# Kernel tuning notes

Measured on AMD Instinct MI355X. Metric: run time of the kernel, lower is better.

Reference implementation:

```python
import jax, jax.numpy as jnp
import numpy as np

HIDDEN = 2048
NUM_HEADS = 16
HEAD_DIM = HIDDEN // NUM_HEADS  # 128
B, S = 2, 2048


def setup_inputs() -> dict:
    key = jax.random.key(0)
    ks = jax.random.split(key, 16)
    w = lambda k, shp: (jax.random.normal(k, shp, jnp.float32) * 0.02)
    return {
        "query": jax.random.normal(ks[0], (B, S, HIDDEN), jnp.float32),
        "key": jax.random.normal(ks[1], (B, S, HIDDEN), jnp.float32),
        "value": jax.random.normal(ks[2], (B, S, HIDDEN), jnp.float32),
        "Wq": w(ks[3], (HIDDEN, HIDDEN)), "bq": jnp.zeros((HIDDEN,), jnp.float32),
        "Wk": w(ks[4], (HIDDEN, HIDDEN)), "bk": jnp.zeros((HIDDEN,), jnp.float32),
        "Wv": w(ks[5], (HIDDEN, HIDDEN)), "bv": jnp.zeros((HIDDEN,), jnp.float32),
        "Wo": w(ks[6], (HIDDEN, HIDDEN)), "bo": jnp.zeros((HIDDEN,), jnp.float32),
        "Wf1": w(ks[7], (HEAD_DIM, 2 * HEAD_DIM)), "bf1": jnp.zeros((2 * HEAD_DIM,), jnp.float32),
        "Wf2": w(ks[8], (2 * HEAD_DIM, HEAD_DIM)), "bf2": jnp.zeros((HEAD_DIM,), jnp.float32),
    }


def reference(query, key, value, Wq, bq, Wk, bk, Wv, bv, Wo, bo, Wf1, bf1, Wf2, bf2):
    b, s, _ = query.shape

    def split_heads(x):  # [b,s,H] -> [b,h,s,d]
        return x.reshape(b, s, NUM_HEADS, HEAD_DIM).transpose(0, 2, 1, 3)

    def feature_map(x):  # MLP on last dim: d -> 2d -> relu -> d
        return jax.nn.relu(x @ Wf1 + bf1) @ Wf2 + bf2

    Q = feature_map(split_heads(query @ Wq + bq))
    K = feature_map(split_heads(key @ Wk + bk))
    V = split_heads(value @ Wv + bv)

    # K^T V per head: [b,h,d,e]
    KV = jnp.einsum("bhsd,bhse->bhde", K, V)
    QKV = jnp.einsum("bhsd,bhde->bhse", Q, KV)
    # denominator: sum of all K entries per (b,h) -> scalar per head
    denom = jnp.sum(K, axis=(-2, -1), keepdims=True) + 1e-8
    QKV = QKV / denom

    context = QKV.transpose(0, 2, 1, 3).reshape(b, s, HIDDEN)
    output = context @ Wo + bo

    attn_weights = jnp.full((b, NUM_HEADS, s, s), 1.0 / s, dtype=query.dtype)
    return output, attn_weights
```

## Files before the change

kernel.cpp:

```cpp
#include <hip/hip_runtime.h>


typedef __bf16 bf16_t;
typedef __bf16 bf16x8 __attribute__((ext_vector_type(8)));
typedef __bf16 bf16x4 __attribute__((ext_vector_type(4)));
typedef float  f32x4  __attribute__((ext_vector_type(4)));

#define FILLV (1.0f / 2048.0f)

#define VMCNT2() asm volatile("s_waitcnt vmcnt(2)" ::: "memory")
#define VMCNT0() asm volatile("s_waitcnt vmcnt(0)" ::: "memory")
#define LGKM0()  asm volatile("s_waitcnt lgkmcnt(0)" ::: "memory")
#define BAR()    __builtin_amdgcn_s_barrier()
#define SCHED0() __builtin_amdgcn_sched_barrier(0)

__device__ __forceinline__ void gload16(const void* g, void* l) {
  __builtin_amdgcn_global_load_lds(
      (__attribute__((address_space(1))) void*)(g),
      (__attribute__((address_space(3))) void*)(l), 16, 0, 0);
}

__device__ __forceinline__ void stage_half(const bf16_t* __restrict__ g,
                                           int h, unsigned char* ldsT, int t) {
  const bf16_t* gh = g + (long)h * 128 * 2048;
  unsigned char* lh = ldsT + h * 16384;
#pragma unroll
  for (int i = 0; i < 2; ++i) {
    const int c = t + i * 512;
    const int r = c >> 3;
    const int cc = ((c & 7) ^ (r & 7)) * 8;
    gload16(gh + (long)r * 2048 + cc, lh + c * 16);
  }
}

__device__ __forceinline__ bf16x8 lds_frag(const unsigned char* base,
                                           int row, int kelem) {
  int byte = row * 128 + kelem * 2;
  byte ^= (row & 7) << 4;
  return *(const bf16x8*)(base + byte);
}

template<bool OUTF32, bool TRIPLE>
__global__ __launch_bounds__(512, 2) void gemm8(
    const bf16_t* __restrict__ A, const bf16_t* __restrict__ Wt,
    const float* __restrict__ b0, const float* __restrict__ b1,
    const float* __restrict__ b2, void* __restrict__ C,
    float* __restrict__ attn, long fillBase)
{
  __shared__ __align__(16) unsigned char smem[98304];
  const int t = threadIdx.x;
  const int lane = t & 63;
  const int wid = t >> 6;
  const int wr = wid >> 2, wc = wid & 3;
  const int bid = blockIdx.x;
  const int nby = gridDim.x >> 4;
  const int by = bid % nby, bx = bid / nby;
  const int which = TRIPLE ? (by >> 4) : 0;
  const bf16_t* Ab = A + (long)by * 256 * 2048;
  const bf16_t* Bb = Wt + (long)which * 4194304 + (long)bx * 128 * 2048;
  const float* bias = TRIPLE ? (which == 0 ? b0 : (which == 1 ? b1 : b2)) : b0;

  const int lr = lane & 15;
  const int l8 = (lane >> 4) * 8;
  const f32x4 fv = {FILLV, FILLV, FILLV, FILLV};
  const int nblk = gridDim.x;

  f32x4 acc[8][2];
#pragma unroll
  for (int i = 0; i < 8; ++i)
#pragma unroll
    for (int j = 0; j < 2; ++j) acc[i][j] = (f32x4){0.f, 0.f, 0.f, 0.f};

  stage_half(Ab, 0, smem, t);
  stage_half(Ab, 1, smem, t);
  stage_half(Bb, 0, smem + 32768, t);

  bf16x8 aF[4][2], bF[2][2];

  for (int kt = 0; kt < 32; ++kt) {
    const int cur = kt & 1;
    unsigned char* curA = smem + cur * 49152;
    unsigned char* curB = curA + 32768;
    unsigned char* nxtA = smem + (cur ^ 1) * 49152;
    unsigned char* nxtB = nxtA + 32768;
    const bool hn = kt < 31;
    const bf16_t* An = Ab + (kt + 1) * 64;
    const bf16_t* Bn = Bb + (kt + 1) * 64;
    const int arow = wr * 128 + lr;
    const int brow = wc * 32 + lr;
    f32x4* fillp = (f32x4*)attn + fillBase + ((long)kt * nblk + bid) * 1024 + t;

    if (hn) { stage_half(An, 0, nxtA, t); VMCNT2(); }
    else    { VMCNT0(); }
    BAR();
#pragma unroll
    for (int mi = 0; mi < 4; ++mi)
#pragma unroll
      for (int kk = 0; kk < 2; ++kk)
        aF[mi][kk] = lds_frag(curA, arow + mi * 16, kk * 32 + l8);
#pragma unroll
    for (int kk = 0; kk < 2; ++kk)
      bF[0][kk] = lds_frag(curB, brow, kk * 32 + l8);
    LGKM0(); SCHED0();
    __builtin_amdgcn_s_setprio(1);
#pragma unroll
    for (int mi = 0; mi < 4; ++mi)
#pragma unroll
      for (int kk = 0; kk < 2; ++kk)
        acc[mi][0] = __builtin_amdgcn_mfma_f32_16x16x32_bf16(
            aF[mi][kk], bF[0][kk], acc[mi][0], 0, 0, 0);
    __builtin_amdgcn_s_setprio(0);
    BAR();

    if (hn) stage_half(An, 1, nxtA, t);
    __builtin_nontemporal_store(fv, fillp);
#pragma unroll
    for (int kk = 0; kk < 2; ++kk)
      bF[1][kk] = lds_frag(curB, brow + 16, kk * 32 + l8);
    BAR(); LGKM0(); SCHED0();
    __builtin_amdgcn_s_setprio(1);
#pragma unroll
    for (int mi = 0; mi < 4; ++mi)
#pragma unroll
      for (int kk = 0; kk < 2; ++kk)
        acc[mi][1] = __builtin_amdgcn_mfma_f32_16x16x32_bf16(
            aF[mi][kk], bF[1][kk], acc[mi][1], 0, 0, 0);
    __builtin_amdgcn_s_setprio(0);
    BAR();

    if (hn) stage_half(Bn, 0, nxtB, t);
    __builtin_nontemporal_store(fv, fillp + 512);
#pragma unroll
    for (int mi = 0; mi < 4; ++mi)
#pragma unroll
      for (int kk = 0; kk < 2; ++kk)
        aF[mi][kk] = lds_frag(curA, arow + 64 + mi * 16, kk * 32 + l8);
    BAR(); LGKM0(); SCHED0();
    __builtin_amdgcn_s_setprio(1);
#pragma unroll
    for (int mi = 0; mi < 4; ++mi)
#pragma unroll
      for (int kk = 0; kk < 2; ++kk)
        acc[4 + mi][0] = __builtin_amdgcn_mfma_f32_16x16x32_bf16(
            aF[mi][kk], bF[0][kk], acc[4 + mi][0], 0, 0, 0);
    __builtin_amdgcn_s_setprio(0);
    BAR();

    BAR(); SCHED0();
    __builtin_amdgcn_s_setprio(1);
#pragma unroll
    for (int mi = 0; mi < 4; ++mi)
#pragma unroll
      for (int kk = 0; kk < 2; ++kk)
        acc[4 + mi][1] = __builtin_amdgcn_mfma_f32_16x16x32_bf16(
            aF[mi][kk], bF[1][kk], acc[4 + mi][1], 0, 0, 0);
    __builtin_amdgcn_s_setprio(0);
    BAR();
  }

  const int row0g = by * 256 + wr * 128;
  const int col0g = bx * 128 + wc * 32;
  float* lw = (float*)smem + wid * 2304;
#pragma unroll
  for (int p = 0; p < 2; ++p) {
    LGKM0();
#pragma unroll
    for (int mi = 0; mi < 4; ++mi)
#pragma unroll
      for (int ni = 0; ni < 2; ++ni) {
        const float bvv = bias[col0g + ni * 16 + lr];
#pragma unroll
        for (int j = 0; j < 4; ++j) {
          const int rl = mi * 16 + (lane >> 4) * 4 + j;
          lw[rl * 36 + ni * 16 + lr] = acc[p * 4 + mi][ni][j] + bvv;
        }
      }
    LGKM0(); SCHED0();
#pragma unroll
    for (int i = 0; i < 8; ++i) {
      const int c = i * 64 + lane;
      const int rl = c >> 3, cc = (c & 7) * 4;
      f32x4 v4 = *(const f32x4*)&lw[rl * 36 + cc];
      const long gaddr = (long)(row0g + p * 64 + rl) * 2048 + col0g + cc;
      if (OUTF32) {
        *(f32x4*)&((float*)C)[gaddr] = v4;
      } else {
        bf16x4 o = {(bf16_t)v4[0], (bf16_t)v4[1],
                    (bf16_t)v4[2], (bf16_t)v4[3]};
        *(bf16x4*)&((bf16_t*)C)[gaddr] = o;
      }
    }
  }
}

__global__ __launch_bounds__(256) void gemm_bt(
    const bf16_t* __restrict__ A, const bf16_t* __restrict__ Bt,
    bf16_t* __restrict__ C, int K, int lda, int ldb, int ldc,
    long aBatchB, long aBatchH, long bBatchB, long bBatchH,
    long cBatchB, long cBatchH, int HperB)
{
  __shared__ bf16_t As[128 * 64];
  __shared__ bf16_t Bs[128 * 64];

  const int z  = blockIdx.z;
  const int zb = z / HperB, zh = z % HperB;
  const bf16_t* Ab = A  + (long)zb * aBatchB + (long)zh * aBatchH
                        + (long)blockIdx.y * 128 * lda;
  const bf16_t* Bb = Bt + (long)zb * bBatchB + (long)zh * bBatchH
                        + (long)blockIdx.x * 128 * ldb;

  const int t = threadIdx.x;
  const int lane = t & 63, w = t >> 6;
  const int wm = (w >> 1) * 64, wn = (w & 1) * 64;

  f32x4 acc[4][4];
#pragma unroll
  for (int i = 0; i < 4; ++i)
#pragma unroll
    for (int j = 0; j < 4; ++j) acc[i][j] = (f32x4){0.f, 0.f, 0.f, 0.f};

  for (int k0 = 0; k0 < K; k0 += 64) {
#pragma unroll
    for (int i = 0; i < 4; ++i) {
      int c = i * 256 + t;
      int row = c >> 3, col = (c & 7) * 8;
      gload16(Ab + (long)row * lda + k0 + col, &As[c * 8]);
      gload16(Bb + (long)row * ldb + k0 + col, &Bs[c * 8]);
    }
    __syncthreads();
#pragma unroll
    for (int kk = 0; kk < 2; ++kk) {
      bf16x8 af[4], bfr[4];
#pragma unroll
      for (int mi = 0; mi < 4; ++mi)
        af[mi] = *(const bf16x8*)&As[(wm + mi * 16 + (lane & 15)) * 64
                                     + kk * 32 + (lane >> 4) * 8];
#pragma unroll
      for (int ni = 0; ni < 4; ++ni)
        bfr[ni] = *(const bf16x8*)&Bs[(wn + ni * 16 + (lane & 15)) * 64
                                      + kk * 32 + (lane >> 4) * 8];
#pragma unroll
      for (int mi = 0; mi < 4; ++mi)
#pragma unroll
        for (int ni = 0; ni < 4; ++ni)
          acc[mi][ni] = __builtin_amdgcn_mfma_f32_16x16x32_bf16(
              af[mi], bfr[ni], acc[mi][ni], 0, 0, 0);
    }
    __syncthreads();
  }

  const long cb = (long)zb * cBatchB + (long)zh * cBatchH;
  const int row0 = blockIdx.y * 128 + wm;
  const int col0 = blockIdx.x * 128 + wn;
#pragma unroll
  for (int mi = 0; mi < 4; ++mi) {
#pragma unroll
    for (int ni = 0; ni < 4; ++ni) {
      const int col = col0 + ni * 16 + (lane & 15);
#pragma unroll
      for (int j = 0; j < 4; ++j) {
        const int row = row0 + mi * 16 + (lane >> 4) * 4 + j;
        C[cb + (long)row * ldc + col] = (bf16_t)acc[mi][ni][j];
      }
    }
  }
}

__global__ __launch_bounds__(256) void fm_fused(
    const bf16_t* __restrict__ A, const bf16_t* __restrict__ W1f,
    const bf16_t* __restrict__ W2f, const float* __restrict__ b1,
    const float* __restrict__ b2, bf16_t* __restrict__ Out)
{
  __shared__ __align__(16) unsigned char As_[16384];
  __shared__ char Hs[64 * 256 * 2];
  const int t = threadIdx.x, lane = t & 63, w = t >> 6;
  const long r0 = (long)blockIdx.x * 64;
  const int lr = lane & 15, lk = lane >> 4;

  {
    const bf16_t* Ab = A + r0 * 128;
#pragma unroll
    for (int i = 0; i < 4; ++i) {
      int c = i * 256 + t;
      int r = c >> 4;
      int cc = ((c & 15) ^ (r & 7)) * 8;
      gload16(Ab + (long)r * 128 + cc, As_ + c * 16);
    }
  }
  __syncthreads();

  f32x4 acc[4][4];
#pragma unroll
  for (int i = 0; i < 4; ++i)
#pragma unroll
    for (int j = 0; j < 4; ++j) acc[i][j] = (f32x4){0.f, 0.f, 0.f, 0.f};
  const int wn = w * 64;
#pragma unroll
  for (int kk = 0; kk < 4; ++kk) {
    bf16x8 af[4], bfr[4];
#pragma unroll
    for (int mi = 0; mi < 4; ++mi) {
      const int m = mi * 16 + lr;
      int byte = (m << 8) + kk * 64 + lk * 16;
      byte ^= (m & 7) << 4;
      af[mi] = *(const bf16x8*)(As_ + byte);
    }
#pragma unroll
    for (int ni = 0; ni < 4; ++ni)
      bfr[ni] = *(const bf16x8*)&W1f[((((w << 2) + ni) << 2) + kk) * 512
                                     + lane * 8];
#pragma unroll
    for (int mi = 0; mi < 4; ++mi)
#pragma unroll
      for (int ni = 0; ni < 4; ++ni)
        acc[mi][ni] = __builtin_amdgcn_mfma_f32_16x16x32_bf16(
            af[mi], bfr[ni], acc[mi][ni], 0, 0, 0);
  }
#pragma unroll
  for (int ni = 0; ni < 4; ++ni) {
    const int col = wn + ni * 16 + lr;
    const float bvv = b1[col];
#pragma unroll
    for (int mi = 0; mi < 4; ++mi)
#pragma unroll
      for (int j = 0; j < 4; ++j) {
        const int row = mi * 16 + lk * 4 + j;
        float h = fmaxf(acc[mi][ni][j] + bvv, 0.f);
        int byte = (row << 9) + (col << 1);
        byte ^= (row & 7) << 4;
        *(bf16_t*)(Hs + byte) = (bf16_t)h;
      }
  }
  __syncthreads();

  f32x4 acc2[4][2];
#pragma unroll
  for (int i = 0; i < 4; ++i)
#pragma unroll
    for (int j = 0; j < 2; ++j) acc2[i][j] = (f32x4){0.f, 0.f, 0.f, 0.f};
  const int wn2 = w * 32;
#pragma unroll
  for (int kk = 0; kk < 8; ++kk) {
    bf16x8 af[4], bfr[2];
#pragma unroll
    for (int mi = 0; mi < 4; ++mi) {
      const int m = mi * 16 + lr;
      int byte = (m << 9) + kk * 64 + lk * 16;
      byte ^= (m & 7) << 4;
      af[mi] = *(const bf16x8*)(Hs + byte);
    }
#pragma unroll
    for (int ni = 0; ni < 2; ++ni)
      bfr[ni] = *(const bf16x8*)&W2f[((((w << 1) + ni) << 3) + kk) * 512
                                     + lane * 8];
#pragma unroll
    for (int mi = 0; mi < 4; ++mi)
#pragma unroll
      for (int ni = 0; ni < 2; ++ni)
        acc2[mi][ni] = __builtin_amdgcn_mfma_f32_16x16x32_bf16(
            af[mi], bfr[ni], acc2[mi][ni], 0, 0, 0);
  }
#pragma unroll
  for (int ni = 0; ni < 2; ++ni) {
    const int col = wn2 + ni * 16 + lr;
    const float bvv = b2[col];
#pragma unroll
    for (int mi = 0; mi < 4; ++mi)
#pragma unroll
      for (int j = 0; j < 4; ++j) {
        const int row = mi * 16 + lk * 4 + j;
        Out[(r0 + row) * 128 + col] = (bf16_t)(acc2[mi][ni][j] + bvv);
      }
  }
}

__global__ __launch_bounds__(256) void prep(
    const float* __restrict__ q, const float* __restrict__ k,
    const float* __restrict__ v,
    const float* __restrict__ Wq, const float* __restrict__ Wk,
    const float* __restrict__ Wv, const float* __restrict__ Wo,
    const float* __restrict__ Wf1, const float* __restrict__ Wf2,
    bf16_t* __restrict__ qkv_bf, bf16_t* __restrict__ Wqkv_t,
    bf16_t* __restrict__ Wf1_f, bf16_t* __restrict__ Wf2_f)
{
  const int t = threadIdx.x;
  const int bid = blockIdx.x;
  __shared__ float ts[64 * 65];

  if (bid < 12288) {
    const float* in = bid < 4096 ? q : (bid < 8192 ? k : v);
    bf16_t* o = qkv_bf + (long)(bid >> 12) * 8388608L;
    const long base = (long)(bid & 4095) * 2048 + t * 8;
    float4 x0 = *(const float4*)&in[base];
    float4 x1 = *(const float4*)&in[base + 4];
    bf16x8 r = {(bf16_t)x0.x, (bf16_t)x0.y, (bf16_t)x0.z, (bf16_t)x0.w,
                (bf16_t)x1.x, (bf16_t)x1.y, (bf16_t)x1.z, (bf16_t)x1.w};
    *(bf16x8*)&o[base] = r;
    return;
  }

  if (bid >= 16384) {
    const bool isW2 = (bid == 16385);
    const float* Wsrc = isW2 ? Wf2 : Wf1;
    bf16_t* dst = isW2 ? Wf2_f : Wf1_f;
    const int Nd2 = isW2 ? 128 : 256;
#pragma unroll
    for (int i = 0; i < 16; ++i) {
      const int idx = t * 16 + i;
      const int ln = idx & 63;
      int kk, col;
      if (!isW2) {
        kk = (idx >> 6) & 3;
        const int ni = (idx >> 8) & 3, ww = idx >> 10;
        col = ww * 64 + ni * 16 + (ln & 15);
      } else {
        kk = (idx >> 6) & 7;
        const int ni = (idx >> 9) & 1, ww = idx >> 10;
        col = ww * 32 + ni * 16 + (ln & 15);
      }
      const int krow = kk * 32 + (ln >> 4) * 8;
      bf16x8 vv;
#pragma unroll
      for (int e = 0; e < 8; ++e)
        vv[e] = (bf16_t)Wsrc[(long)(krow + e) * Nd2 + col];
      *(bf16x8*)&dst[(long)idx * 8] = vv;
    }
    return;
  }

  const int tile = bid - 12288;
  const int wsel = tile >> 10, r = tile & 1023;
  const float* W = wsel == 0 ? Wq : wsel == 1 ? Wk : wsel == 2 ? Wv : Wo;
  bf16_t* outp = Wqkv_t + (long)wsel * 4194304L;
  const int k0 = (r >> 5) * 64, n0 = (r & 31) * 64;

#pragma unroll
  for (int i = 0; i < 4; ++i) {
    const int idx = i * 256 + t;
    const int rr = idx >> 4, cc = (idx & 15) * 4;
    float4 x = *(const float4*)&W[(long)(k0 + rr) * 2048 + n0 + cc];
    float* p = &ts[rr * 65 + cc];
    p[0] = x.x; p[1] = x.y; p[2] = x.z; p[3] = x.w;
  }
  __syncthreads();

#pragma unroll
  for (int i = 0; i < 2; ++i) {
    const int idx = i * 256 + t;
    const int n = idx >> 3, kc = (idx & 7) * 8;
    bf16x8 vv;
#pragma unroll
    for (int qq = 0; qq < 8; ++qq) vv[qq] = (bf16_t)ts[(kc + qq) * 65 + n];
    *(bf16x8*)&outp[(long)(n0 + n) * 2048 + k0 + kc] = vv;
  }
}

__global__ __launch_bounds__(256) void kv_partial(
    const bf16_t* __restrict__ Kf, const bf16_t* __restrict__ Vp,
    float* __restrict__ part, float* __restrict__ part_denom) {
  const int z = blockIdx.y, b = z >> 4, h = z & 15;
  const int s0 = blockIdx.x * 256;
  const int t = threadIdx.x;
  __shared__ bf16_t Ks[32 * 128];
  __shared__ bf16_t Vs[32 * 128];
  __shared__ float red[4];
  const bf16_t* Kb = Kf + (long)b * 4194304 + h * 128;
  const bf16_t* Vb = Vp + (long)b * 4194304 + h * 128;
  float acc[8][8];
#pragma unroll
  for (int i = 0; i < 8; ++i)
#pragma unroll
    for (int j = 0; j < 8; ++j) acc[i][j] = 0.f;
  float ksum = 0.f;
  const int d0 = (t & 15) * 8, e0 = (t >> 4) * 8;
  for (int sc = 0; sc < 256; sc += 32) {
#pragma unroll
    for (int i = 0; i < 2; ++i) {
      int idx = (i * 256 + t) * 8;
      int r = idx >> 7, c = idx & 127;
      long g = (long)(s0 + sc + r) * 2048 + c;
      *(bf16x8*)&Ks[r * 128 + c] = *(const bf16x8*)&Kb[g];
      *(bf16x8*)&Vs[r * 128 + c] = *(const bf16x8*)&Vb[g];
    }
    __syncthreads();
    {
      bf16x8 a0 = *(const bf16x8*)&Ks[t * 16];
      bf16x8 a1 = *(const bf16x8*)&Ks[t * 16 + 8];
#pragma unroll
      for (int j = 0; j < 8; ++j) ksum += (float)a0[j] + (float)a1[j];
    }
    for (int s = 0; s < 32; ++s) {
      bf16x8 kv = *(const bf16x8*)&Ks[s * 128 + d0];
      bf16x8 vv = *(const bf16x8*)&Vs[s * 128 + e0];
      float kf[8], vf[8];
#pragma unroll
      for (int i = 0; i < 8; ++i) { kf[i] = (float)kv[i]; vf[i] = (float)vv[i]; }
#pragma unroll
      for (int i = 0; i < 8; ++i)
#pragma unroll
        for (int j = 0; j < 8; ++j) acc[i][j] += vf[i] * kf[j];
    }
    __syncthreads();
  }

#pragma unroll
  for (int off = 32; off; off >>= 1) ksum += __shfl_down(ksum, off, 64);
  if ((t & 63) == 0) red[t >> 6] = ksum;
  __syncthreads();
  if (t == 0)
    part_denom[blockIdx.x * 32 + z] = red[0] + red[1] + red[2] + red[3];

  float* pb = part + ((long)blockIdx.x * 32 + z) * 16384;
#pragma unroll
  for (int i = 0; i < 8; ++i)
#pragma unroll
    for (int j = 0; j < 8; ++j)
      pb[(e0 + i) * 128 + (d0 + j)] = acc[i][j];
}

__global__ __launch_bounds__(256) void kv_reduce(
    const float* __restrict__ part, const float* __restrict__ part_denom,
    bf16_t* __restrict__ KVT) {
  const int z = blockIdx.x >> 4, slice = blockIdx.x & 15;
  const int t = threadIdx.x;
  float dsum = 0.f;
#pragma unroll
  for (int c = 0; c < 8; ++c) dsum += part_denom[c * 32 + z];
  const float inv = 1.0f / (dsum + 1e-8f);
  const long i0 = slice * 1024 + t * 4;
  f32x4 s = {0.f, 0.f, 0.f, 0.f};
#pragma unroll
  for (int c = 0; c < 8; ++c) {
    f32x4 v = *(const f32x4*)&part[((long)c * 32 + z) * 16384 + i0];
    s.x += v.x; s.y += v.y; s.z += v.z; s.w += v.w;
  }
  bf16x4 o = {(bf16_t)(s.x * inv), (bf16_t)(s.y * inv),
              (bf16_t)(s.z * inv), (bf16_t)(s.w * inv)};
  *(bf16x4*)&KVT[(long)z * 16384 + i0] = o;
}

extern "C" void kernel_launch(void* const* d_in, const int* in_sizes, int n_in,
                              void* d_out, int out_size, void* d_ws, size_t ws_size,
                              hipStream_t stream) {
  (void)in_sizes; (void)n_in; (void)out_size; (void)ws_size;
  const float* q   = (const float*)d_in[0];
  const float* k   = (const float*)d_in[1];
  const float* v   = (const float*)d_in[2];
  const float* Wq  = (const float*)d_in[3];
  const float* bq  = (const float*)d_in[4];
  const float* Wk  = (const float*)d_in[5];
  const float* bk  = (const float*)d_in[6];
  const float* Wv  = (const float*)d_in[7];
  const float* bv  = (const float*)d_in[8];
  const float* Wo  = (const float*)d_in[9];
  const float* bo  = (const float*)d_in[10];
  const float* Wf1 = (const float*)d_in[11];
  const float* bf1 = (const float*)d_in[12];
  const float* Wf2 = (const float*)d_in[13];
  const float* bf2 = (const float*)d_in[14];

  bf16_t* P      = (bf16_t*)d_ws;
  bf16_t* qkv_bf = P;
  bf16_t* Wqkv_t = P + 25165824L;
  bf16_t* Wo_t   = P + 37748736L;
  bf16_t* Qp     = P + 42008576L;
  bf16_t* Vp     = P + 58785792L;
  bf16_t* Qf     = P + 83951616L;
  bf16_t* Kf     = P + 92340224L;
  bf16_t* KVT    = P + 100728832L;
  bf16_t* Wf1_f  = P + 101253120L;
  bf16_t* Wf2_f  = P + 101285888L;
  float*  part   = (float*)d_ws;
  float*  part_denom = (float*)d_ws + 4194304L;

  float* out0 = (float*)d_out;
  float* attn = (float*)d_out + 8388608L;

  dim3 blk(256);

  prep<<<16386, blk, 0, stream>>>(q, k, v, Wq, Wk, Wv, Wo, Wf1, Wf2,
                                  qkv_bf, Wqkv_t, Wf1_f, Wf2_f);

  gemm8<false, true><<<768, 512, 0, stream>>>(
      qkv_bf, Wqkv_t, bq, bk, bv, Qp, attn, 0L);

  fm_fused<<<2048, blk, 0, stream>>>(Qp, Wf1_f, Wf2_f, bf1, bf2, Qf);

  kv_partial<<<dim3(8, 32), blk, 0, stream>>>(Kf, Vp, part, part_denom);

  kv_reduce<<<512, blk, 0, stream>>>(part, part_denom, KVT);

  gemm_bt<<<dim3(1, 16, 32), blk, 0, stream>>>(
      Qf, KVT, Vp, 128, 2048, 128, 2048,
      4194304L, 128L, 262144L, 16384L, 4194304L, 128L, 16);

  gemm8<true, false><<<256, 512, 0, stream>>>(
      Vp, Wo_t, bo, nullptr, nullptr, out0, attn, 25165824L);
}
```

Before: 299.8 us.

## Fuse feature-map MLP into QKV projection GEMM epilogue

The QKV projection GEMM and the separate feature-map MLP kernel are merged into one kernel. Q and K tiles (256 tokens × 128 head-dim) stay in LDS, where the two-layer MLP runs directly and the result is written to Qf/Kf. The V tiles keep the plain epilogue. This removes the Qp round trip through global memory and one kernel launch. In exchange, LDS grows to 128KB and launch bounds drop to one block per CU, which lowers occupancy during the main GEMM loop.

```diff
diff --git a/kernel.cpp b/kernel.cpp
--- a/kernel.cpp
+++ b/kernel.cpp
@@ -40,11 +40,273 @@
   return *(const bf16x8*)(base + byte);
 }
 
-template<bool OUTF32, bool TRIPLE>
-__global__ __launch_bounds__(512, 2) void gemm8(
+__global__ __launch_bounds__(512, 1) void proj_fm8(
     const bf16_t* __restrict__ A, const bf16_t* __restrict__ Wt,
-    const float* __restrict__ b0, const float* __restrict__ b1,
-    const float* __restrict__ b2, void* __restrict__ C,
+    const float* __restrict__ bq, const float* __restrict__ bk,
+    const float* __restrict__ bv,
+    const bf16_t* __restrict__ W1f, const bf16_t* __restrict__ W2f,
+    const float* __restrict__ b1, const float* __restrict__ b2,
+    bf16_t* __restrict__ Vp, bf16_t* __restrict__ Qf, bf16_t* __restrict__ Kf,
+    float* __restrict__ attn)
+{
+  __shared__ __align__(16) unsigned char smem[131072];
+  const int t = threadIdx.x;
+  const int lane = t & 63;
+  const int wid = t >> 6;
+  const int wr = wid >> 2, wc = wid & 3;
+  const int bid = blockIdx.x;
+  const int by = bid % 48, bx = bid / 48;
+  const int which = by >> 4;
+  const bf16_t* Ab = A + (long)by * 256 * 2048;
+  const bf16_t* Bb = Wt + (long)which * 4194304 + (long)bx * 128 * 2048;
+  const float* bias = which == 0 ? bq : (which == 1 ? bk : bv);
+
+  const int lr = lane & 15;
+  const int l8 = (lane >> 4) * 8;
+  const f32x4 fv = {FILLV, FILLV, FILLV, FILLV};
+
+  f32x4 acc[8][2];
+#pragma unroll
+  for (int i = 0; i < 8; ++i)
+#pragma unroll
+    for (int j = 0; j < 2; ++j) acc[i][j] = (f32x4){0.f, 0.f, 0.f, 0.f};
+
+  stage_half(Ab, 0, smem, t);
+  stage_half(Ab, 1, smem, t);
+  stage_half(Bb, 0, smem + 32768, t);
+
+  bf16x8 aF[4][2], bF[2][2];
+
+  for (int kt = 0; kt < 32; ++kt) {
+    const int cur = kt & 1;
+    unsigned char* curA = smem + cur * 49152;
+    unsigned char* curB = curA + 32768;
+    unsigned char* nxtA = smem + (cur ^ 1) * 49152;
+    unsigned char* nxtB = nxtA + 32768;
+    const bool hn = kt < 31;
+    const bf16_t* An = Ab + (kt + 1) * 64;
+    const bf16_t* Bn = Bb + (kt + 1) * 64;
+    const int arow = wr * 128 + lr;
+    const int brow = wc * 32 + lr;
+    f32x4* fillp = (f32x4*)attn + ((long)kt * 768 + bid) * 1024 + t;
+
+    if (hn) { stage_half(An, 0, nxtA, t); VMCNT2(); }
+    else    { VMCNT0(); }
+    BAR();
+#pragma unroll
+    for (int mi = 0; mi < 4; ++mi)
+#pragma unroll
+      for (int kk = 0; kk < 2; ++kk)
+        aF[mi][kk] = lds_frag(curA, arow + mi * 16, kk * 32 + l8);
+#pragma unroll
+    for (int kk = 0; kk < 2; ++kk)
+      bF[0][kk] = lds_frag(curB, brow, kk * 32 + l8);
+    LGKM0(); SCHED0();
+    __builtin_amdgcn_s_setprio(1);
+#pragma unroll
+    for (int mi = 0; mi < 4; ++mi)
+#pragma unroll
+      for (int kk = 0; kk < 2; ++kk)
+        acc[mi][0] = __builtin_amdgcn_mfma_f32_16x16x32_bf16(
+            aF[mi][kk], bF[0][kk], acc[mi][0], 0, 0, 0);
+    __builtin_amdgcn_s_setprio(0);
+    BAR();
+
+    if (hn) stage_half(An, 1, nxtA, t);
+    __builtin_nontemporal_store(fv, fillp);
+#pragma unroll
+    for (int kk = 0; kk < 2; ++kk)
+      bF[1][kk] = lds_frag(curB, brow + 16, kk * 32 + l8);
+    BAR(); LGKM0(); SCHED0();
+    __builtin_amdgcn_s_setprio(1);
+#pragma unroll
+    for (int mi = 0; mi < 4; ++mi)
+#pragma unroll
+      for (int kk = 0; kk < 2; ++kk)
+        acc[mi][1] = __builtin_amdgcn_mfma_f32_16x16x32_bf16(
+            aF[mi][kk], bF[1][kk], acc[mi][1], 0, 0, 0);
+    __builtin_amdgcn_s_setprio(0);
+    BAR();
+
+    if (hn) stage_half(Bn, 0, nxtB, t);
+    __builtin_nontemporal_store(fv, fillp + 512);
+#pragma unroll
+    for (int mi = 0; mi < 4; ++mi)
+#pragma unroll
+      for (int kk = 0; kk < 2; ++kk)
+        aF[mi][kk] = lds_frag(curA, arow + 64 + mi * 16, kk * 32 + l8);
+    BAR(); LGKM0(); SCHED0();
+    __builtin_amdgcn_s_setprio(1);
+#pragma unroll
+    for (int mi = 0; mi < 4; ++mi)
+#pragma unroll
+      for (int kk = 0; kk < 2; ++kk)
+        acc[4 + mi][0] = __builtin_amdgcn_mfma_f32_16x16x32_bf16(
+            aF[mi][kk], bF[0][kk], acc[4 + mi][0], 0, 0, 0);
+    __builtin_amdgcn_s_setprio(0);
+    BAR();
+
+    BAR(); SCHED0();
+    __builtin_amdgcn_s_setprio(1);
+#pragma unroll
+    for (int mi = 0; mi < 4; ++mi)
+#pragma unroll
+      for (int kk = 0; kk < 2; ++kk)
+        acc[4 + mi][1] = __builtin_amdgcn_mfma_f32_16x16x32_bf16(
+            aF[mi][kk], bF[1][kk], acc[4 + mi][1], 0, 0, 0);
+    __builtin_amdgcn_s_setprio(0);
+    BAR();
+  }
+
+  const int tokBase = (by & 15) * 256;
+  const int col0 = wc * 32;
+
+  if (which == 2) {
+    float* lw = (float*)smem + wid * 2304;
+#pragma unroll
+    for (int p = 0; p < 2; ++p) {
+      LGKM0();
+#pragma unroll
+      for (int mi = 0; mi < 4; ++mi)
+#pragma unroll
+        for (int ni = 0; ni < 2; ++ni) {
+          const float bvv = bias[bx * 128 + col0 + ni * 16 + lr];
+#pragma unroll
+          for (int j = 0; j < 4; ++j) {
+            const int rl = mi * 16 + (lane >> 4) * 4 + j;
+            lw[rl * 36 + ni * 16 + lr] = acc[p * 4 + mi][ni][j] + bvv;
+          }
+        }
+      LGKM0(); SCHED0();
+#pragma unroll
+      for (int i = 0; i < 8; ++i) {
+        const int c = i * 64 + lane;
+        const int rl = c >> 3, cc = (c & 7) * 4;
+        f32x4 v4 = *(const f32x4*)&lw[rl * 36 + cc];
+        const int tok = tokBase + wr * 128 + p * 64 + rl;
+        bf16x4 o = {(bf16_t)v4[0], (bf16_t)v4[1],
+                    (bf16_t)v4[2], (bf16_t)v4[3]};
+        *(bf16x4*)&Vp[(long)tok * 2048 + bx * 128 + col0 + cc] = o;
+      }
+    }
+    return;
+  }
+
+  unsigned char* Ct = smem;
+  unsigned char* Hs = smem + 65536;
+
+#pragma unroll
+  for (int mi = 0; mi < 8; ++mi)
+#pragma unroll
+    for (int ni = 0; ni < 2; ++ni) {
+      const int col = col0 + ni * 16 + lr;
+      const float bvv = bias[bx * 128 + col];
+#pragma unroll
+      for (int j = 0; j < 4; ++j) {
+        const int row = wr * 128 + mi * 16 + (lane >> 4) * 4 + j;
+        int byte = (row << 8) + (col << 1);
+        byte ^= (row & 7) << 4;
+        *(bf16_t*)(Ct + byte) = (bf16_t)(acc[mi][ni][j] + bvv);
+      }
+    }
+  __syncthreads();
+
+  bf16_t* dst = which == 0 ? Qf : Kf;
+  const int wr2 = wid >> 2, wc2 = wid & 3;
+  const int lk = lane >> 4;
+
+#pragma unroll
+  for (int p = 0; p < 2; ++p) {
+    f32x4 a1[4][4];
+#pragma unroll
+    for (int i = 0; i < 4; ++i)
+#pragma unroll
+      for (int j = 0; j < 4; ++j) a1[i][j] = (f32x4){0.f, 0.f, 0.f, 0.f};
+#pragma unroll
+    for (int kk = 0; kk < 4; ++kk) {
+      bf16x8 af[4], bfr[4];
+#pragma unroll
+      for (int mi = 0; mi < 4; ++mi) {
+        const int row = p * 128 + wr2 * 64 + mi * 16 + lr;
+        int byte = (row << 8) + (kk * 64 + lk * 16);
+        byte ^= (row & 7) << 4;
+        af[mi] = *(const bf16x8*)(Ct + byte);
+      }
+#pragma unroll
+      for (int ni = 0; ni < 4; ++ni)
+        bfr[ni] = *(const bf16x8*)&W1f[((((wc2 << 2) + ni) << 2) + kk) * 512
+                                       + lane * 8];
+#pragma unroll
+      for (int mi = 0; mi < 4; ++mi)
+#pragma unroll
+        for (int ni = 0; ni < 4; ++ni)
+          a1[mi][ni] = __builtin_amdgcn_mfma_f32_16x16x32_bf16(
+              af[mi], bfr[ni], a1[mi][ni], 0, 0, 0);
+    }
+    if (p) __syncthreads();
+#pragma unroll
+    for (int ni = 0; ni < 4; ++ni) {
+      const int col = wc2 * 64 + ni * 16 + lr;
+      const float bvv = b1[col];
+#pragma unroll
+      for (int mi = 0; mi < 4; ++mi)
+#pragma unroll
+        for (int j = 0; j < 4; ++j) {
+          const int row = wr2 * 64 + mi * 16 + lk * 4 + j;
+          float h = fmaxf(a1[mi][ni][j] + bvv, 0.f);
+          int byte = (row << 9) + (col << 1);
+          byte ^= (row & 7) << 4;
+          *(bf16_t*)(Hs + byte) = (bf16_t)h;
+        }
+    }
+    __syncthreads();
+
+    f32x4 a2[4][2];
+#pragma unroll
+    for (int i = 0; i < 4; ++i)
+#pragma unroll
+      for (int j = 0; j < 2; ++j) a2[i][j] = (f32x4){0.f, 0.f, 0.f, 0.f};
+#pragma unroll
+    for (int kk = 0; kk < 8; ++kk) {
+      bf16x8 af[4], bfr[2];
+#pragma unroll
+      for (int mi = 0; mi < 4; ++mi) {
+        const int row = wr2 * 64 + mi * 16 + lr;
+        int byte = (row << 9) + (kk * 64 + lk * 16);
+        byte ^= (row & 7) << 4;
+        af[mi] = *(const bf16x8*)(Hs + byte);
+      }
+#pragma unroll
+      for (int ni = 0; ni < 2; ++ni)
+        bfr[ni] = *(const bf16x8*)&W2f[((((wc2 << 1) + ni) << 3) + kk) * 512
+                                       + lane * 8];
+#pragma unroll
+      for (int mi = 0; mi < 4; ++mi)
+#pragma unroll
+        for (int ni = 0; ni < 2; ++ni)
+          a2[mi][ni] = __builtin_amdgcn_mfma_f32_16x16x32_bf16(
+              af[mi], bfr[ni], a2[mi][ni], 0, 0, 0);
+    }
+#pragma unroll
+    for (int ni = 0; ni < 2; ++ni) {
+      const int col = wc2 * 32 + ni * 16 + lr;
+      const float bvv = b2[col];
+#pragma unroll
+      for (int mi = 0; mi < 4; ++mi)
+#pragma unroll
+        for (int j = 0; j < 4; ++j) {
+          const int rl = wr2 * 64 + mi * 16 + lk * 4 + j;
+          const int tok = tokBase + p * 128 + rl;
+          dst[(long)tok * 2048 + bx * 128 + col] =
+              (bf16_t)(a2[mi][ni][j] + bvv);
+        }
+    }
+  }
+}
+
+__global__ __launch_bounds__(512, 2) void gemm8out(
+    const bf16_t* __restrict__ A, const bf16_t* __restrict__ Wt,
+    const float* __restrict__ b0, float* __restrict__ C,
     float* __restrict__ attn, long fillBase)
 {
   __shared__ __align__(16) unsigned char smem[98304];
@@ -55,10 +317,8 @@
   const int bid = blockIdx.x;
   const int nby = gridDim.x >> 4;
   const int by = bid % nby, bx = bid / nby;
-  const int which = TRIPLE ? (by >> 4) : 0;
   const bf16_t* Ab = A + (long)by * 256 * 2048;
-  const bf16_t* Bb = Wt + (long)which * 4194304 + (long)bx * 128 * 2048;
-  const float* bias = TRIPLE ? (which == 0 ? b0 : (which == 1 ? b1 : b2)) : b0;
+  const bf16_t* Bb = Wt + (long)bx * 128 * 2048;
 
   const int lr = lane & 15;
   const int l8 = (lane >> 4) * 8;
@@ -168,7 +428,7 @@
     for (int mi = 0; mi < 4; ++mi)
 #pragma unroll
       for (int ni = 0; ni < 2; ++ni) {
-        const float bvv = bias[col0g + ni * 16 + lr];
+        const float bvv = b0[col0g + ni * 16 + lr];
 #pragma unroll
         for (int j = 0; j < 4; ++j) {
           const int rl = mi * 16 + (lane >> 4) * 4 + j;
@@ -181,14 +441,7 @@
       const int c = i * 64 + lane;
       const int rl = c >> 3, cc = (c & 7) * 4;
       f32x4 v4 = *(const f32x4*)&lw[rl * 36 + cc];
-      const long gaddr = (long)(row0g + p * 64 + rl) * 2048 + col0g + cc;
-      if (OUTF32) {
-        *(f32x4*)&((float*)C)[gaddr] = v4;
-      } else {
-        bf16x4 o = {(bf16_t)v4[0], (bf16_t)v4[1],
-                    (bf16_t)v4[2], (bf16_t)v4[3]};
-        *(bf16x4*)&((bf16_t*)C)[gaddr] = o;
-      }
+      *(f32x4*)&C[(long)(row0g + p * 64 + rl) * 2048 + col0g + cc] = v4;
     }
   }
 }
@@ -263,114 +516,6 @@
         C[cb + (long)row * ldc + col] = (bf16_t)acc[mi][ni][j];
       }
     }
-  }
-}
-
-__global__ __launch_bounds__(256) void fm_fused(
-    const bf16_t* __restrict__ A, const bf16_t* __restrict__ W1f,
-    const bf16_t* __restrict__ W2f, const float* __restrict__ b1,
-    const float* __restrict__ b2, bf16_t* __restrict__ Out)
-{
-  __shared__ __align__(16) unsigned char As_[16384];
-  __shared__ char Hs[64 * 256 * 2];
-  const int t = threadIdx.x, lane = t & 63, w = t >> 6;
-  const long r0 = (long)blockIdx.x * 64;
-  const int lr = lane & 15, lk = lane >> 4;
-
-  {
-    const bf16_t* Ab = A + r0 * 128;
-#pragma unroll
-    for (int i = 0; i < 4; ++i) {
-      int c = i * 256 + t;
-      int r = c >> 4;
-      int cc = ((c & 15) ^ (r & 7)) * 8;
-      gload16(Ab + (long)r * 128 + cc, As_ + c * 16);
-    }
-  }
-  __syncthreads();
-
-  f32x4 acc[4][4];
-#pragma unroll
-  for (int i = 0; i < 4; ++i)
-#pragma unroll
-    for (int j = 0; j < 4; ++j) acc[i][j] = (f32x4){0.f, 0.f, 0.f, 0.f};
-  const int wn = w * 64;
-#pragma unroll
-  for (int kk = 0; kk < 4; ++kk) {
-    bf16x8 af[4], bfr[4];
-#pragma unroll
-    for (int mi = 0; mi < 4; ++mi) {
-      const int m = mi * 16 + lr;
-      int byte = (m << 8) + kk * 64 + lk * 16;
-      byte ^= (m & 7) << 4;
-      af[mi] = *(const bf16x8*)(As_ + byte);
-    }
-#pragma unroll
-    for (int ni = 0; ni < 4; ++ni)
-      bfr[ni] = *(const bf16x8*)&W1f[((((w << 2) + ni) << 2) + kk) * 512
-                                     + lane * 8];
-#pragma unroll
-    for (int mi = 0; mi < 4; ++mi)
-#pragma unroll
-      for (int ni = 0; ni < 4; ++ni)
-        acc[mi][ni] = __builtin_amdgcn_mfma_f32_16x16x32_bf16(
-            af[mi], bfr[ni], acc[mi][ni], 0, 0, 0);
-  }
-#pragma unroll
-  for (int ni = 0; ni < 4; ++ni) {
-    const int col = wn + ni * 16 + lr;
-    const float bvv = b1[col];
-#pragma unroll
-    for (int mi = 0; mi < 4; ++mi)
-#pragma unroll
-      for (int j = 0; j < 4; ++j) {
-        const int row = mi * 16 + lk * 4 + j;
-        float h = fmaxf(acc[mi][ni][j] + bvv, 0.f);
-        int byte = (row << 9) + (col << 1);
-        byte ^= (row & 7) << 4;
-        *(bf16_t*)(Hs + byte) = (bf16_t)h;
-      }
-  }
-  __syncthreads();
-
-  f32x4 acc2[4][2];
-#pragma unroll
-  for (int i = 0; i < 4; ++i)
-#pragma unroll
-    for (int j = 0; j < 2; ++j) acc2[i][j] = (f32x4){0.f, 0.f, 0.f, 0.f};
-  const int wn2 = w * 32;
-#pragma unroll
-  for (int kk = 0; kk < 8; ++kk) {
-    bf16x8 af[4], bfr[2];
-#pragma unroll
-    for (int mi = 0; mi < 4; ++mi) {
-      const int m = mi * 16 + lr;
-      int byte = (m << 9) + kk * 64 + lk * 16;
-      byte ^= (m & 7) << 4;
-      af[mi] = *(const bf16x8*)(Hs + byte);
-    }
-#pragma unroll
-    for (int ni = 0; ni < 2; ++ni)
-      bfr[ni] = *(const bf16x8*)&W2f[((((w << 1) + ni) << 3) + kk) * 512
-                                     + lane * 8];
-#pragma unroll
-    for (int mi = 0; mi < 4; ++mi)
-#pragma unroll
-      for (int ni = 0; ni < 2; ++ni)
-        acc2[mi][ni] = __builtin_amdgcn_mfma_f32_16x16x32_bf16(
-            af[mi], bfr[ni], acc2[mi][ni], 0, 0, 0);
-  }
-#pragma unroll
-  for (int ni = 0; ni < 2; ++ni) {
-    const int col = wn2 + ni * 16 + lr;
-    const float bvv = b2[col];
-#pragma unroll
-    for (int mi = 0; mi < 4; ++mi)
-#pragma unroll
-      for (int j = 0; j < 4; ++j) {
-        const int row = mi * 16 + lk * 4 + j;
-        Out[(r0 + row) * 128 + col] = (bf16_t)(acc2[mi][ni][j] + bvv);
-      }
   }
 }
 
@@ -563,7 +708,6 @@
   bf16_t* qkv_bf = P;
   bf16_t* Wqkv_t = P + 25165824L;
   bf16_t* Wo_t   = P + 37748736L;
-  bf16_t* Qp     = P + 42008576L;
   bf16_t* Vp     = P + 58785792L;
   bf16_t* Qf     = P + 83951616L;
   bf16_t* Kf     = P + 92340224L;
@@ -581,10 +725,9 @@
   prep<<<16386, blk, 0, stream>>>(q, k, v, Wq, Wk, Wv, Wo, Wf1, Wf2,
                                   qkv_bf, Wqkv_t, Wf1_f, Wf2_f);
 
-  gemm8<false, true><<<768, 512, 0, stream>>>(
-      qkv_bf, Wqkv_t, bq, bk, bv, Qp, attn, 0L);
-
-  fm_fused<<<2048, blk, 0, stream>>>(Qp, Wf1_f, Wf2_f, bf1, bf2, Qf);
+  proj_fm8<<<768, 512, 0, stream>>>(
+      qkv_bf, Wqkv_t, bq, bk, bv, Wf1_f, Wf2_f, bf1, bf2,
+      Vp, Qf, Kf, attn);
 
   kv_partial<<<dim3(8, 32), blk, 0, stream>>>(Kf, Vp, part, part_denom);
 
@@ -594,6 +737,5 @@
       Qf, KVT, Vp, 128, 2048, 128, 2048,
       4194304L, 128L, 262144L, 16384L, 4194304L, 128L, 16);
 
-  gemm8<true, false><<<256, 512, 0, stream>>>(
-      Vp, Wo_t, bo, nullptr, nullptr, out0, attn, 25165824L);
-}
+  gemm8out<<<256, 512, 0, stream>>>(Vp, Wo_t, bo, out0, attn, 25165824L);
+}
```

New measurement: 353.6 us. 18.0% more time.
